# Performance work log

Measured on AMD Instinct MI355X. Metric: run time of the kernel, lower is better.

The kernel has to match this reference:

```python
import jax, jax.numpy as jnp
import numpy as np

GRAPH_BIAS_SCALE = 0.8
CTX_GATE_STRENGTH = 2.0
COMMITMENT_COST = 0.25
DECAY = 0.99

N = 262144      # flattened batch*seq tokens
LAT = 128       # latent_dim
DIM = 2 * LAT   # concat(real, imag)
K_SYN = 64
K_SEM = 128


def setup_inputs() -> dict:
    key = jax.random.key(0)
    ks = jax.random.split(key, 18)
    f = jnp.float32
    return {
        "z_fast_re": jax.random.normal(ks[0], (N, LAT), f),
        "z_fast_im": jax.random.normal(ks[1], (N, LAT), f),
        "z_slow_re": jax.random.normal(ks[2], (N, LAT), f),
        "z_slow_im": jax.random.normal(ks[3], (N, LAT), f),
        "cb_syn": jax.random.normal(ks[4], (K_SYN, DIM), f),
        "cb_sem": jax.random.normal(ks[5], (K_SEM, DIM), f),
        "W_syn": jax.random.normal(ks[6], (DIM, K_SYN), f) / np.sqrt(DIM),
        "b_syn": jnp.zeros((K_SYN,), f),
        "W_sem": jax.random.normal(ks[7], (DIM, K_SEM), f) / np.sqrt(DIM),
        "b_sem": jnp.zeros((K_SEM,), f),
        "cl_syn": jnp.zeros((K_SYN,), f),
        "avg_syn": jax.random.normal(ks[8], (K_SYN, DIM), f),
        "cl_sem": jnp.zeros((K_SEM,), f),
        "avg_sem": jax.random.normal(ks[9], (K_SEM, DIM), f),
        "adj_syn": jnp.zeros((K_SYN, K_SYN), f),
        "adj_sem": jnp.zeros((K_SEM, K_SEM), f),
        "prev_syn": jax.random.randint(ks[10], (N,), 0, K_SYN, jnp.int32),
        "prev_sem": jax.random.randint(ks[11], (N,), 0, K_SEM, jnp.int32),
    }


def _vq_step(z_re, z_im, cb, W, b, cl, avg, adj, prev):
    """One context-gated VQ step (training mode). Returns straight-through
    quantized flat latent, loss, indices, and the updated buffers/codebook."""
    K = cb.shape[0]
    zf = jnp.concatenate([z_re, z_im], axis=-1)          # [N, DIM]
    # squared-distance matrix [N, K]
    d = (jnp.sum(zf * zf, axis=1, keepdims=True)
         + jnp.sum(cb * cb, axis=1)
         - 2.0 * zf @ cb.T)
    bias_history = jax.nn.sigmoid(adj[prev])             # [N, K] gather
    bias_context = jax.nn.softmax(zf @ W + b, axis=-1)   # [N, K]
    d = d - (GRAPH_BIAS_SCALE * bias_history + CTX_GATE_STRENGTH * bias_context)
    idx = jnp.argmin(d, axis=1)                          # [N]
    z_q = cb[idx]                                        # [N, DIM] gather
    adj_new = adj.at[prev, idx].set(adj[prev, idx] * 0.995 + 1.0)
    # EMA codebook update (uses detached stats; mutates after z_q already gathered)
    counts = jnp.zeros((K,), zf.dtype).at[idx].add(1.0)          # enc.sum(0)
    embed_sum = jnp.zeros((K, zf.shape[1]), zf.dtype).at[idx].add(zf)  # enc.T @ zf
    cl_new = cl * DECAY + (1.0 - DECAY) * counts
    avg_new = avg * DECAY + (1.0 - DECAY) * embed_sum
    n = jnp.sum(cl_new)
    cs = (cl_new + 1e-6) / (n + K * 1e-6) * n
    cb_new = avg_new / cs[:, None]
    # losses use z_q from the OLD codebook (gathered before the EMA copy)
    sg = jax.lax.stop_gradient
    loss = (jnp.mean((sg(z_q) - zf) ** 2)
            + COMMITMENT_COST * jnp.mean((z_q - sg(zf)) ** 2))
    zq_st = zf + sg(z_q - zf)                            # straight-through
    return zq_st, loss, idx, cl_new, avg_new, cb_new, adj_new


def reference(z_fast_re, z_fast_im, z_slow_re, z_slow_im,
              cb_syn, cb_sem, W_syn, b_syn, W_sem, b_sem,
              cl_syn, avg_syn, cl_sem, avg_sem, adj_syn, adj_sem,
              prev_syn, prev_sem):
    zq_syn, loss_syn, idx_syn, cl_syn_n, avg_syn_n, cb_syn_n, adj_syn_n = _vq_step(
        z_fast_re, z_fast_im, cb_syn, W_syn, b_syn, cl_syn, avg_syn, adj_syn, prev_syn)
    zq_sem, loss_sem, idx_sem, cl_sem_n, avg_sem_n, cb_sem_n, adj_sem_n = _vq_step(
        z_slow_re, z_slow_im, cb_sem, W_sem, b_sem, cl_sem, avg_sem, adj_sem, prev_sem)
    # zq_* are the flat (real||imag) representation of the complex outputs
    return (zq_syn, zq_sem, loss_syn + loss_sem, idx_syn, idx_sem,
            cb_syn_n, cl_syn_n, avg_syn_n, adj_syn_n,
            cb_sem_n, cl_sem_n, avg_sem_n, adj_sem_n)
```

## Files before the change

kernel.cpp:

```cpp
#include <hip/hip_runtime.h>

#define N_TOK 262144
#define LATD  128
#define DIMD  256

using f32x4  = __attribute__((ext_vector_type(4)))  float;
using f32x16 = __attribute__((ext_vector_type(16))) float;
using f16x8  = __attribute__((ext_vector_type(8)))  _Float16;
using f16x2  = __attribute__((ext_vector_type(2)))  _Float16;

#define W_PACK_SYN 0
#define W_PACK_SEM 32768
#define W_CBN_SYN  98304
#define W_CBN_SEM  98368
#define W_IDX_SYN  98496
#define W_IDX_SEM  360640
#define W_CNT_SYN  622784
#define W_CNT_SEM  622848
#define W_EMB_SYN  622976
#define W_EMB_SEM  639360
#define W_MRK_SYN  672128
#define W_MRK_SEM  676224
#define W_LOSSP_SYN 692612
#define W_LOSSP_SEM 700804
#define W_ZERO_BEG 622784
#define W_ZERO_END 692612

#define OFF_ZQ_SYN  0LL
#define OFF_ZQ_SEM  67108864LL
#define OFF_LOSS    134217728LL
#define OFF_IDX_SYN 134217729LL
#define OFF_IDX_SEM 134479873LL
#define OFF_CB_SYN  134742017LL
#define OFF_CL_SYN  134758401LL
#define OFF_AVG_SYN 134758465LL
#define OFF_ADJ_SYN 134774849LL
#define OFF_CB_SEM  134778945LL
#define OFF_CL_SEM  134811713LL
#define OFF_AVG_SEM 134811841LL
#define OFF_ADJ_SEM 134844609LL

__device__ inline void gload16(const void* g, void* l) {
  __builtin_amdgcn_global_load_lds(
      (const __attribute__((address_space(1))) unsigned int*)g,
      (__attribute__((address_space(3))) unsigned int*)l, 16, 0, 0);
}

template <int K>
__device__ void prep_pack_body(int bid2, const float* __restrict__ cb,
                               const float* __restrict__ W, _Float16* __restrict__ pack) {
  constexpr int NCT = 2 * K / 32;
  constexpr int PER_KT = NCT * 512;
  int t = bid2 * 256 + threadIdx.x;
  int kt = t / PER_KT;
  int r  = t - kt * PER_KT;
  int l  = (r >> 3) & 63;
  int e  = r & 7;
  int ct = r >> 9;
  int j   = kt * 16 + (l >> 5) * 8 + e;
  int col = ct * 32 + (l & 31);
  float x = (col < K) ? cb[col * DIMD + j] : W[j * K + (col - K)];
  _Float16 h = (_Float16)x;
  _Float16 lo = (_Float16)(x - (float)h);
  pack[(size_t)kt * 2 * PER_KT + r]          = h;
  pack[(size_t)kt * 2 * PER_KT + PER_KT + r] = lo;
}

__global__ __launch_bounds__(256) void k_prep(
    const float* __restrict__ cbs, const float* __restrict__ cbm,
    const float* __restrict__ Wsy, const float* __restrict__ Wse,
    float* __restrict__ ws, _Float16* __restrict__ packs, _Float16* __restrict__ packm) {
  __shared__ float red[256];
  const int bid = blockIdx.x, tid = threadIdx.x;
  if (bid < 273) {
    int idx = W_ZERO_BEG + bid * 256 + tid;
    if (idx < W_ZERO_END) ws[idx] = 0.0f;
  } else if (bid < 401) {
    prep_pack_body<64>(bid - 273, cbs, Wsy, packs);
  } else if (bid < 657) {
    prep_pack_body<128>(bid - 401, cbm, Wse, packm);
  } else {
    int k = bid - 657;
    const float* src; float* dst;
    if (k < 64) { src = cbs + (size_t)k * DIMD; dst = ws + W_CBN_SYN + k; }
    else        { src = cbm + (size_t)(k - 64) * DIMD; dst = ws + W_CBN_SEM + (k - 64); }
    float v = src[tid];
    red[tid] = v * v;
    __syncthreads();
    for (int s = 128; s > 0; s >>= 1) {
      if (tid < s) red[tid] += red[tid + s];
      __syncthreads();
    }
    if (tid == 0) *dst = red[0];
  }
}

template <int K>
__global__ __launch_bounds__(256, 2) void k_passA(
    const float* __restrict__ zre, const float* __restrict__ zim,
    const _Float16* __restrict__ pack, const float* __restrict__ cbn,
    const float* __restrict__ cb,  const float* __restrict__ bvec,
    const float* __restrict__ adj, const int* __restrict__ prev,
    float* __restrict__ zq_out, float* __restrict__ idxf_out,
    int* __restrict__ idxi_ws, int* __restrict__ mark_ws,
    float* __restrict__ lossp) {
  constexpr int NCT = K / 16;
  constexpr int NH  = K / 32;
  constexpr int PER_KT = NCT * 512;
  constexpr int CHUNK = 2 * PER_KT;
  constexpr int SITERS = CHUNK * 2 / 4096;
  __shared__ __align__(16) _Float16 packl[2 * CHUNK];
  __shared__ float wred[4];

  const int tid  = threadIdx.x;
  const int lane = tid & 63;
  const int wv   = tid >> 6;
  const int kg   = lane >> 5;
  const int j    = lane & 31;
  const int t0   = blockIdx.x * 128 + wv * 32;
  const int gt   = t0 + j;

  auto stage = [&](int kt) {
    const _Float16* src = pack + (size_t)kt * CHUNK;
    char* dst = (char*)packl + (kt & 1) * CHUNK * 2;
#pragma unroll
    for (int i = 0; i < SITERS; ++i)
      gload16(src + (size_t)(i * 256 + tid) * 8,
              dst + ((i * 256 + (tid & 192)) << 4));
  };

  f32x16 acc[NCT];
#pragma unroll
  for (int t = 0; t < NCT; ++t)
#pragma unroll
    for (int r = 0; r < 16; ++r) acc[t][r] = 0.0f;
  float zn = 0.0f;

  stage(0);
  f32x4 v0, v1, nv0, nv1;
  {
    const float* zp = zre + (size_t)gt * LATD + kg * 8;
    v0 = *(const f32x4*)zp;
    v1 = *(const f32x4*)(zp + 4);
  }
  for (int kt = 0; kt < 16; ++kt) {
    __syncthreads();
    if (kt + 1 < 16) stage(kt + 1);
    if (kt + 1 < 16) {
      const float* zsrc2 = (kt + 1 < 8) ? zre : zim;
      const float* zp2 = zsrc2 + (size_t)gt * LATD + ((kt + 1) & 7) * 16 + kg * 8;
      nv0 = *(const f32x4*)zp2;
      nv1 = *(const f32x4*)(zp2 + 4);
    }
    f16x8 Bh, Bl;
#pragma unroll
    for (int e = 0; e < 4; ++e) {
      _Float16 h0 = (_Float16)v0[e];
      Bh[e] = h0;       Bl[e] = (_Float16)(v0[e] - (float)h0);
      _Float16 h1 = (_Float16)v1[e];
      Bh[e + 4] = h1;   Bl[e + 4] = (_Float16)(v1[e] - (float)h1);
      zn += v0[e] * v0[e];
      zn += v1[e] * v1[e];
    }
    const _Float16* Bp = packl + (kt & 1) * CHUNK;
#pragma unroll
    for (int t = 0; t < NCT; ++t) {
      f16x8 Ah = *(const f16x8*)(Bp + (size_t)t * 512 + lane * 8);
      f16x8 Al = *(const f16x8*)(Bp + PER_KT + (size_t)t * 512 + lane * 8);
      acc[t] = __builtin_amdgcn_mfma_f32_32x32x16_f16(Ah, Bh, acc[t], 0, 0, 0);
      acc[t] = __builtin_amdgcn_mfma_f32_32x32x16_f16(Ah, Bl, acc[t], 0, 0, 0);
      acc[t] = __builtin_amdgcn_mfma_f32_32x32x16_f16(Al, Bh, acc[t], 0, 0, 0);
    }
    v0 = nv0; v1 = nv1;
  }

  const int pv = prev[gt];

  float mx = -1e30f;
#pragma unroll
  for (int t = 0; t < NH; ++t)
#pragma unroll
    for (int q = 0; q < 4; ++q) {
      f32x4 bv4 = *(const f32x4*)&bvec[t * 32 + 8 * q + 4 * kg];
#pragma unroll
      for (int b = 0; b < 4; ++b) {
        acc[NH + t][4 * q + b] += bv4[b];
        mx = fmaxf(mx, acc[NH + t][4 * q + b]);
      }
    }
  mx = fmaxf(mx, __shfl_xor(mx, 32));
  float es = 0.0f;
#pragma unroll
  for (int t = 0; t < NH; ++t)
#pragma unroll
    for (int r = 0; r < 16; ++r) {
      acc[NH + t][r] = __expf(acc[NH + t][r] - mx);
      es += acc[NH + t][r];
    }
  es += __shfl_xor(es, 32);
  const float inv = 1.0f / es;

  const float* adjrow = adj + (size_t)pv * K;
  float best = -1e30f; int bidx = 0; float bdot = 0.0f;
#pragma unroll
  for (int t = 0; t < NH; ++t)
#pragma unroll
    for (int q = 0; q < 4; ++q) {
      const int e0 = t * 32 + 8 * q + 4 * kg;
      f32x4 cb4v = *(const f32x4*)&cbn[e0];
      f32x4 ad4  = *(const f32x4*)&adjrow[e0];
#pragma unroll
      for (int b = 0; b < 4; ++b) {
        int r = 4 * q + b;
        float dot = acc[t][r];
        float sg  = 1.0f / (1.0f + __expf(-ad4[b]));
        float sc  = dot - 0.5f * cb4v[b] + 0.4f * sg + acc[NH + t][r] * inv;
        int   e   = e0 + b;
        if (sc > best || (sc == best && e < bidx)) {
          best = sc; bidx = e; bdot = dot;
        }
      }
    }
  {
    float ob = __shfl_xor(best, 32);
    int   oi = __shfl_xor(bidx, 32);
    float od = __shfl_xor(bdot, 32);
    if (ob > best || (ob == best && oi < bidx)) { best = ob; bidx = oi; bdot = od; }
  }
  const float znf = zn + __shfl_xor(zn, 32);

  float lj = 0.0f;
  if (lane < 32) {
    idxf_out[gt] = (float)bidx;
    idxi_ws[gt]  = bidx;
    mark_ws[pv * K + bidx] = 1;
    lj = cbn[bidx] + znf - 2.0f * bdot;
  }
#pragma unroll
  for (int off = 32; off; off >>= 1) lj += __shfl_xor(lj, off);
  if (lane == 0) wred[wv] = lj;

  const float4* cb4p = (const float4*)cb;
  float4* zq4 = (float4*)zq_out;
#pragma unroll 4
  for (int i = 0; i < 32; ++i) {
    int bi_i = __shfl(bidx, i);
    zq4[(size_t)(t0 + i) * 64 + lane] = cb4p[(size_t)bi_i * 64 + lane];
  }
  __syncthreads();
  if (tid == 0) lossp[blockIdx.x] = wred[0] + wred[1] + wred[2] + wred[3];
}

template <int K>
__device__ void passB_body(int fid,
    const float* __restrict__ zre, const float* __restrict__ zim,
    const int* __restrict__ idxi,
    float* __restrict__ emb_ws, int* __restrict__ cnt_ws,
    int* idxl, int* cntl, unsigned short* zT) {
  constexpr int TPB  = 2048;
  constexpr int CH   = 128;
  constexpr int NCT2 = (K == 64) ? 1 : 2;
  const int tid  = threadIdx.x;
  const int lane = tid & 63, wv = tid >> 6;
  const int cg    = fid & 3;
  const int chunk = fid >> 2;
  const int tbase = chunk * TPB;

  if (tid < K) cntl[tid] = 0;
  __syncthreads();
#pragma unroll
  for (int i = 0; i < TPB / 256; ++i) {
    int id = idxi[tbase + i * 256 + tid];
    idxl[i * 256 + tid] = id;
    if (cg == 0) atomicAdd(&cntl[id], 1);
  }
  __syncthreads();
  if (cg == 0 && tid < K) atomicAdd(&cnt_ws[tid], cntl[tid]);

  const int rt  = (K == 64) ? (wv & 1) : wv;
  const int ct0 = (K == 64) ? (wv >> 1) : 0;
  const int krow = rt * 32 + (lane & 31);
  const int kg   = lane >> 5;
  const float* zsrc = (cg < 2) ? zre : zim;
  const int cbase = (cg & 1) * 64;

  f32x16 acc[NCT2];
#pragma unroll
  for (int c = 0; c < NCT2; ++c)
#pragma unroll
    for (int r = 0; r < 16; ++r) acc[c][r] = 0.0f;

  const int sq = tid & 15;
  const int sp = tid >> 4;

  auto stage = [&](int sc) {
    unsigned short* zb = zT + (sc & 1) * 8192;
#pragma unroll
    for (int it = 0; it < 4; ++it) {
      int p = sp + it * 16;
      int t = sc * CH + 2 * p;
      const float* zr = zsrc + (size_t)(tbase + t) * LATD + cbase + 4 * sq;
      f32x4 a = *(const f32x4*)zr;
      f32x4 b = *(const f32x4*)(zr + LATD);
#pragma unroll
      for (int c4 = 0; c4 < 4; ++c4) {
        int c = 4 * sq + c4;
        f16x2 pr;
        pr[0] = (_Float16)a[c4];
        pr[1] = (_Float16)b[c4];
        int byte = c * 256 + ((4 * p) ^ ((c & 7) << 4));
        *(f16x2*)((char*)zb + byte) = pr;
      }
    }
  };

  stage(0);
  for (int sc = 0; sc < TPB / CH; ++sc) {
    __syncthreads();
    if (sc + 1 < TPB / CH) stage(sc + 1);
    const unsigned short* zb = zT + (sc & 1) * 8192;
#pragma unroll
    for (int st = 0; st < 8; ++st) {
      const int tloc = sc * CH + st * 16 + kg * 8;
      f16x8 Af;
#pragma unroll
      for (int e = 0; e < 8; ++e)
        Af[e] = (idxl[tloc + e] == krow) ? (_Float16)1.0f : (_Float16)0.0f;
#pragma unroll
      for (int c = 0; c < NCT2; ++c) {
        int col = (ct0 + c) * 32 + (lane & 31);
        int byte = col * 256 + ((st * 32 + kg * 16) ^ ((col & 7) << 4));
        f16x8 Bf = *(const f16x8*)((const char*)zb + byte);
        acc[c] = __builtin_amdgcn_mfma_f32_32x32x16_f16(Af, Bf, acc[c], 0, 0, 0);
      }
    }
  }
#pragma unroll
  for (int c = 0; c < NCT2; ++c)
#pragma unroll
    for (int r = 0; r < 16; ++r) {
      int row = rt * 32 + (r & 3) + 8 * (r >> 2) + 4 * (lane >> 5);
      int col = cg * 64 + (ct0 + c) * 32 + (lane & 31);
      atomicAdd(&emb_ws[row * DIMD + col], acc[c][r]);
    }
}

__global__ __launch_bounds__(256) void k_passB_all(
    const float* __restrict__ zfre, const float* __restrict__ zfim,
    const float* __restrict__ zsre, const float* __restrict__ zsim,
    const int* __restrict__ idxis, const int* __restrict__ idxim,
    float* __restrict__ embs, float* __restrict__ embm,
    int* __restrict__ cnts, int* __restrict__ cntm) {
  __shared__ int idxl[2048];
  __shared__ int cntl[128];
  __shared__ __align__(16) unsigned short zT[2 * 8192];
  const int fid = blockIdx.x >> 1;
  if ((blockIdx.x & 1) == 0)
    passB_body<64>(fid, zfre, zfim, idxis, embs, cnts, idxl, cntl, zT);
  else
    passB_body<128>(fid, zsre, zsim, idxim, embm, cntm, idxl, cntl, zT);
}

__global__ __launch_bounds__(256) void k_fin(
    const float* __restrict__ ws, const float* __restrict__ clsi, const float* __restrict__ clmi,
    const float* __restrict__ avgs, const float* __restrict__ avgm,
    const float* __restrict__ adjs, const float* __restrict__ adjm,
    float* __restrict__ o_loss, float* __restrict__ o_cl_syn, float* __restrict__ o_cl_sem,
    float* __restrict__ o_cb_syn, float* __restrict__ o_avg_syn, float* __restrict__ o_adj_syn,
    float* __restrict__ o_cb_sem, float* __restrict__ o_avg_sem, float* __restrict__ o_adj_sem) {
  __shared__ float sred[256];
  const int* wsi = (const int*)ws;
  const int bid = blockIdx.x, tid = threadIdx.x;
  if (bid == 0) {
    float s = 0.0f;
    for (int i = tid; i < 2048; i += 256) s += ws[W_LOSSP_SYN + i];
    for (int i = tid; i < 2048; i += 256) s += ws[W_LOSSP_SEM + i];
    sred[tid] = s;
    __syncthreads();
    for (int st = 128; st > 0; st >>= 1) {
      if (tid < st) sred[tid] += sred[tid + st];
      __syncthreads();
    }
    if (tid < 64)
      o_cl_syn[tid] = clsi[tid] * 0.99f + 0.01f * (float)wsi[W_CNT_SYN + tid];
    if (tid < 128)
      o_cl_sem[tid] = clmi[tid] * 0.99f + 0.01f * (float)wsi[W_CNT_SEM + tid];
    if (tid == 0)
      *o_loss = 1.25f * sred[0] / ((float)N_TOK * 256.0f);
    return;
  }
  const int e = (bid - 1) * 256 + tid;
  float n = 0.0f;
  if (e < 49152) {
    const bool syn = e < 16384;
    const int KK = syn ? 64 : 128;
    const float* clp = syn ? clsi : clmi;
    const int cntoff = syn ? W_CNT_SYN : W_CNT_SEM;
    float v = 0.0f;
    if (tid < KK) v = clp[tid] * 0.99f + 0.01f * (float)wsi[cntoff + tid];
    sred[tid] = v;
    __syncthreads();
    for (int st = 128; st > 0; st >>= 1) {
      if (tid < st) sred[tid] += sred[tid + st];
      __syncthreads();
    }
    n = sred[0];
  }
  if (e < 16384) {
    int k = e >> 8;
    float av = avgs[e] * 0.99f + 0.01f * ws[W_EMB_SYN + e];
    o_avg_syn[e] = av;
    float cnt = (float)wsi[W_CNT_SYN + k];
    float cl  = clsi[k] * 0.99f + 0.01f * cnt;
    float cs  = (cl + 1e-6f) / (n + (float)(64 * 1e-6)) * n;
    o_cb_syn[e] = av / cs;
  } else if (e < 49152) {
    int e2 = e - 16384;
    int k = e2 >> 8;
    float av = avgm[e2] * 0.99f + 0.01f * ws[W_EMB_SEM + e2];
    o_avg_sem[e2] = av;
    float cnt = (float)wsi[W_CNT_SEM + k];
    float cl  = clmi[k] * 0.99f + 0.01f * cnt;
    float cs  = (cl + 1e-6f) / (n + (float)(128 * 1e-6)) * n;
    o_cb_sem[e2] = av / cs;
  } else if (e < 53248) {
    int a = e - 49152;
    float old = adjs[a];
    o_adj_syn[a] = wsi[W_MRK_SYN + a] ? old * 0.995f + 1.0f : old;
  } else if (e < 69632) {
    int a = e - 53248;
    float old = adjm[a];
    o_adj_sem[a] = wsi[W_MRK_SEM + a] ? old * 0.995f + 1.0f : old;
  }
}

extern "C" void kernel_launch(void* const* d_in, const int* in_sizes, int n_in,
                              void* d_out, int out_size, void* d_ws, size_t ws_size,
                              hipStream_t stream) {
  const float* zfre = (const float*)d_in[0];
  const float* zfim = (const float*)d_in[1];
  const float* zsre = (const float*)d_in[2];
  const float* zsim = (const float*)d_in[3];
  const float* cbs  = (const float*)d_in[4];
  const float* cbm  = (const float*)d_in[5];
  const float* Wsy  = (const float*)d_in[6];
  const float* bsy  = (const float*)d_in[7];
  const float* Wse  = (const float*)d_in[8];
  const float* bse  = (const float*)d_in[9];
  const float* clsi = (const float*)d_in[10];
  const float* avgs = (const float*)d_in[11];
  const float* clmi = (const float*)d_in[12];
  const float* avgm = (const float*)d_in[13];
  const float* adjs = (const float*)d_in[14];
  const float* adjm = (const float*)d_in[15];
  const int*   prvs = (const int*)d_in[16];
  const int*   prvm = (const int*)d_in[17];

  float* out = (float*)d_out;
  float* wsf = (float*)d_ws;
  int*   wsi = (int*)d_ws;
  _Float16* wsh = (_Float16*)d_ws;

  k_prep<<<849, 256, 0, stream>>>(cbs, cbm, Wsy, Wse, wsf,
      wsh + 2 * W_PACK_SYN, wsh + 2 * W_PACK_SEM);

  k_passA<64><<<N_TOK / 128, 256, 0, stream>>>(
      zfre, zfim, wsh + 2 * W_PACK_SYN, wsf + W_CBN_SYN, cbs, bsy, adjs, prvs,
      out + OFF_ZQ_SYN, out + OFF_IDX_SYN, wsi + W_IDX_SYN, wsi + W_MRK_SYN,
      wsf + W_LOSSP_SYN);
  k_passA<128><<<N_TOK / 128, 256, 0, stream>>>(
      zsre, zsim, wsh + 2 * W_PACK_SEM, wsf + W_CBN_SEM, cbm, bse, adjm, prvm,
      out + OFF_ZQ_SEM, out + OFF_IDX_SEM, wsi + W_IDX_SEM, wsi + W_MRK_SEM,
      wsf + W_LOSSP_SEM);

  k_passB_all<<<1024, 256, 0, stream>>>(
      zfre, zfim, zsre, zsim,
      wsi + W_IDX_SYN, wsi + W_IDX_SEM,
      wsf + W_EMB_SYN, wsf + W_EMB_SEM,
      wsi + W_CNT_SYN, wsi + W_CNT_SEM);

  k_fin<<<273, 256, 0, stream>>>(wsf, clsi, clmi, avgs, avgm, adjs, adjm,
      out + OFF_LOSS, out + OFF_CL_SYN, out + OFF_CL_SEM,
      out + OFF_CB_SYN, out + OFF_AVG_SYN, out + OFF_ADJ_SYN,
      out + OFF_CB_SEM, out + OFF_AVG_SEM, out + OFF_ADJ_SEM);
}
```

Baseline: 505.7 us.

## Stage z tiles through swizzled LDS with async loads; raise occupancy for K=64

The per-thread register prefetch of z rows for the next k-tile is replaced by async global-to-LDS loads of a 128-token z tile, double-buffered alongside the codebook pack. The tile uses an XOR swizzle to avoid bank conflicts, and each lane then reads its 8 floats from LDS. The K=64 instantiation also raises its launch-bounds minimum blocks per CU from 2 to 3. This is meant to make the z loads coalesced, overlap them with the MFMA work, and free registers. In exchange it uses 16 KB more LDS per block and adds LDS traffic, and the tighter register cap could cause spills.

```diff
diff --git a/kernel.cpp b/kernel.cpp
--- a/kernel.cpp
+++ b/kernel.cpp
@@ -96,7 +96,7 @@
 }
 
 template <int K>
-__global__ __launch_bounds__(256, 2) void k_passA(
+__global__ __launch_bounds__(256, (K == 64) ? 3 : 2) void k_passA(
     const float* __restrict__ zre, const float* __restrict__ zim,
     const _Float16* __restrict__ pack, const float* __restrict__ cbn,
     const float* __restrict__ cb,  const float* __restrict__ bvec,
@@ -109,7 +109,8 @@
   constexpr int PER_KT = NCT * 512;
   constexpr int CHUNK = 2 * PER_KT;
   constexpr int SITERS = CHUNK * 2 / 4096;
-  __shared__ __align__(16) _Float16 packl[2 * CHUNK];
+  constexpr int PBYTES = CHUNK * 2;
+  __shared__ __align__(16) char smem[2 * PBYTES + 2 * 8192];
   __shared__ float wred[4];
 
   const int tid  = threadIdx.x;
@@ -119,14 +120,26 @@
   const int j    = lane & 31;
   const int t0   = blockIdx.x * 128 + wv * 32;
   const int gt   = t0 + j;
+  char* zl = smem + 2 * PBYTES;
 
   auto stage = [&](int kt) {
     const _Float16* src = pack + (size_t)kt * CHUNK;
-    char* dst = (char*)packl + (kt & 1) * CHUNK * 2;
+    char* dst = smem + (kt & 1) * PBYTES;
 #pragma unroll
     for (int i = 0; i < SITERS; ++i)
       gload16(src + (size_t)(i * 256 + tid) * 8,
               dst + ((i * 256 + (tid & 192)) << 4));
+    const float* zsrc = (kt < 8) ? zre : zim;
+    const int ktoff = (kt & 7) * 16;
+    char* zdst = zl + (kt & 1) * 8192;
+#pragma unroll
+    for (int it = 0; it < 2; ++it) {
+      int idx = it * 256 + tid;
+      int tok = idx >> 2;
+      int sq  = (idx & 3) ^ ((tok >> 1) & 3);
+      const float* g = zsrc + (size_t)(blockIdx.x * 128 + tok) * LATD + ktoff + sq * 4;
+      gload16(g, zdst + ((it * 256 + (tid & 192)) << 4));
+    }
   };
 
   f32x16 acc[NCT];
@@ -137,21 +150,14 @@
   float zn = 0.0f;
 
   stage(0);
-  f32x4 v0, v1, nv0, nv1;
-  {
-    const float* zp = zre + (size_t)gt * LATD + kg * 8;
-    v0 = *(const f32x4*)zp;
-    v1 = *(const f32x4*)(zp + 4);
-  }
+  const int ltok = wv * 32 + j;
+  const int zs   = (ltok >> 1) & 3;
   for (int kt = 0; kt < 16; ++kt) {
     __syncthreads();
     if (kt + 1 < 16) stage(kt + 1);
-    if (kt + 1 < 16) {
-      const float* zsrc2 = (kt + 1 < 8) ? zre : zim;
-      const float* zp2 = zsrc2 + (size_t)gt * LATD + ((kt + 1) & 7) * 16 + kg * 8;
-      nv0 = *(const f32x4*)zp2;
-      nv1 = *(const f32x4*)(zp2 + 4);
-    }
+    const char* zb = zl + (kt & 1) * 8192;
+    f32x4 v0 = *(const f32x4*)(zb + (ltok * 4 + ((2 * kg)     ^ zs)) * 16);
+    f32x4 v1 = *(const f32x4*)(zb + (ltok * 4 + ((2 * kg + 1) ^ zs)) * 16);
     f16x8 Bh, Bl;
 #pragma unroll
     for (int e = 0; e < 4; ++e) {
@@ -162,7 +168,7 @@
       zn += v0[e] * v0[e];
       zn += v1[e] * v1[e];
     }
-    const _Float16* Bp = packl + (kt & 1) * CHUNK;
+    const _Float16* Bp = (const _Float16*)(smem + (kt & 1) * PBYTES);
 #pragma unroll
     for (int t = 0; t < NCT; ++t) {
       f16x8 Ah = *(const f16x8*)(Bp + (size_t)t * 512 + lane * 8);
@@ -171,7 +177,6 @@
       acc[t] = __builtin_amdgcn_mfma_f32_32x32x16_f16(Ah, Bl, acc[t], 0, 0, 0);
       acc[t] = __builtin_amdgcn_mfma_f32_32x32x16_f16(Al, Bh, acc[t], 0, 0, 0);
     }
-    v0 = nv0; v1 = nv1;
   }
 
   const int pv = prev[gt];
```

After: 540.2 us. +6.8%, slower.
